# Optimization experiments

Hardware: AMD Instinct MI355X
Metric: run time of the kernel (lower is better)

The kernel has to match this reference:

```python
import jax, jax.numpy as jnp
import numpy as np


def conv1x1(x, w, b):
    # x: [B, Cin, H, W], w: [Cout, Cin], b: [Cout]
    return jnp.einsum('oc,bchw->bohw', w, x) + b[None, :, None, None]


def setup_inputs() -> dict:
    key = jax.random.key(0)
    ks = jax.random.split(key, 10)
    B, C, H, W = 8, 256, 64, 64
    C2 = C // 2
    s = 1.0 / np.sqrt(C)
    s2 = 1.0 / np.sqrt(C2)
    return {
        'x1': jax.random.normal(ks[0], (B, C, H, W), jnp.float32),
        'x2': jax.random.normal(ks[1], (B, C, H, W), jnp.float32),
        'w_th': jax.random.uniform(ks[2], (C2, C), jnp.float32, -s, s),
        'b_th': jax.random.uniform(ks[3], (C2,), jnp.float32, -s, s),
        'w_pi': jax.random.uniform(ks[4], (C2, C), jnp.float32, -s, s),
        'b_pi': jax.random.uniform(ks[5], (C2,), jnp.float32, -s, s),
        'w_g': jax.random.uniform(ks[6], (C2, C), jnp.float32, -s, s),
        'b_g': jax.random.uniform(ks[7], (C2,), jnp.float32, -s, s),
        'w_out': jax.random.uniform(ks[8], (C, C2), jnp.float32, -s2, s2),
        'b_out': jax.random.uniform(ks[9], (C,), jnp.float32, -s2, s2),
    }


def reference(x1, x2, w_th, b_th, w_pi, b_pi, w_g, b_g, w_out, b_out):
    B, C, H, W = x1.shape
    HW = H * W
    res = x1
    # 1x1 conv projections -> [B, C2, HW]
    e1 = conv1x1(x1, w_th, b_th).reshape(B, -1, HW)  # theta
    e2 = conv1x1(x2, w_pi, b_pi).reshape(B, -1, HW)  # phi
    # scores: [B, HW, HW]
    f = jnp.einsum('bcq,bck->bqk', e1, e2)
    # GLOBAL softmax over the whole HWxHW matrix per batch element
    f = jax.nn.softmax(f.reshape(B, HW * HW), axis=1).reshape(B, HW, HW)
    g2 = conv1x1(x2, w_g, b_g).reshape(B, -1, HW)  # [B, C2, HW]
    # out = f @ g2^T -> [B, HW, C2] -> [B, C2, H, W]
    out = jnp.einsum('bqk,bck->bcq', f, g2).reshape(B, -1, H, W)
    out = conv1x1(out, w_out, b_out)
    return out + res
```

## Files before the change

### kernel.cpp

```cpp
#include <hip/hip_runtime.h>

typedef unsigned short u16;
typedef unsigned int u32;
typedef short s16x8 __attribute__((ext_vector_type(8)));
typedef float f32x4 __attribute__((ext_vector_type(4)));

#define HWN 4096
#define CC  256
#define C2  128
#define LOG2E 1.4426950408889634f

static __device__ __forceinline__ u16 f2bf(float f) {
    union { float f; u32 u; } c; c.f = f;
    u32 u = c.u;
    u32 r = (u + 0x7fffu + ((u >> 16) & 1u)) >> 16;
    return (u16)r;
}
static __device__ __forceinline__ float bf2f(u16 u) {
    union { u32 u; float f; } c; c.u = ((u32)u) << 16; return c.f;
}
static __device__ __forceinline__ u32 cvtpk(float lo, float hi) {
    u32 d;
    asm("v_cvt_pk_bf16_f32 %0, %1, %2" : "=v"(d) : "v"(lo), "v"(hi));
    return d;
}
static __device__ __forceinline__ float fexp2(float x) {
    return __builtin_amdgcn_exp2f(x);
}

__global__ __launch_bounds__(256) void k_wcvt(
    const float* __restrict__ w_th, const float* __restrict__ w_pi,
    const float* __restrict__ w_g,  const float* __restrict__ w_out,
    u16* __restrict__ wthb, u16* __restrict__ wpib,
    u16* __restrict__ wgb,  u16* __restrict__ woutb)
{
    int i = blockIdx.x * 256 + threadIdx.x;
    wthb[i]  = f2bf(w_th[i] * LOG2E);
    wpib[i]  = f2bf(w_pi[i]);
    wgb[i]   = f2bf(w_g[i]);
    woutb[i] = f2bf(w_out[i]);
}

__device__ __forceinline__ void load_afrag(const float* __restrict__ px, int g, s16x8 a[8]) {
    #pragma unroll
    for (int ks = 0; ks < 8; ++ks) {
        union { s16x8 v; u16 u[8]; } c;
        #pragma unroll
        for (int j = 0; j < 8; ++j)
            c.u[j] = f2bf(px[(size_t)(ks*32 + g*8 + j) * HWN]);
        a[ks] = c.v;
    }
}

__device__ __forceinline__ void proj_gemm(const s16x8 a[8], const u16* __restrict__ wb,
                                          const float* __restrict__ bias, float bscale,
                                          int m16, int g, f32x4 acc[8]) {
    #pragma unroll
    for (int nb = 0; nb < 8; ++nb) {
        float bv = bias[nb*16 + m16] * bscale;
        acc[nb] = (f32x4){bv, bv, bv, bv};
    }
    #pragma unroll
    for (int ks = 0; ks < 8; ++ks) {
        #pragma unroll
        for (int nb = 0; nb < 8; ++nb) {
            s16x8 bb = *(const s16x8*)&wb[(size_t)(nb*16 + m16)*CC + ks*32 + g*8];
            acc[nb] = __builtin_amdgcn_mfma_f32_16x16x32_bf16(a[ks], bb, acc[nb], 0, 0, 0);
        }
    }
}

__global__ __launch_bounds__(256) void k_projM(
    const float* __restrict__ x1, const float* __restrict__ x2,
    const u16* __restrict__ wthb, const float* __restrict__ b_th,
    const u16* __restrict__ wpib, const float* __restrict__ b_pi,
    const u16* __restrict__ wgb,  const float* __restrict__ b_g,
    u16* __restrict__ e1t, u16* __restrict__ e2t, u16* __restrict__ g2t)
{
    __shared__ u16 gs[C2][72];
    const int tid  = threadIdx.x;
    const int b    = blockIdx.x >> 6;
    const int q0   = (blockIdx.x & 63) * 64;
    const int wid  = __builtin_amdgcn_readfirstlane(tid >> 6);
    const int lane = tid & 63;
    const int m16  = lane & 15;
    const int g    = lane >> 4;

    s16x8 a[8];
    f32x4 acc[8];

    const float* px1 = x1 + (size_t)b*CC*HWN + q0 + wid*16 + m16;
    load_afrag(px1, g, a);
    proj_gemm(a, wthb, b_th, LOG2E, m16, g, acc);
    #pragma unroll
    for (int nb = 0; nb < 8; ++nb)
        #pragma unroll
        for (int r = 0; r < 4; ++r)
            e1t[((size_t)b*HWN + q0 + wid*16 + g*4 + r)*C2 + nb*16 + m16] = f2bf(acc[nb][r]);

    const float* px2 = x2 + (size_t)b*CC*HWN + q0 + wid*16 + m16;
    load_afrag(px2, g, a);
    proj_gemm(a, wpib, b_pi, 1.f, m16, g, acc);
    #pragma unroll
    for (int nb = 0; nb < 8; ++nb)
        #pragma unroll
        for (int r = 0; r < 4; ++r) {
            int q   = q0 + wid*16 + g*4 + r;
            int gix = (nb*2 + (m16 >> 3)) ^ (q & 7);
            e2t[((size_t)b*HWN + q)*C2 + gix*8 + (m16 & 7)] = f2bf(acc[nb][r]);
        }

    proj_gemm(a, wgb, b_g, 1.f, m16, g, acc);
    #pragma unroll
    for (int nb = 0; nb < 8; ++nb)
        #pragma unroll
        for (int r = 0; r < 4; ++r)
            gs[nb*16 + m16][wid*16 + g*4 + r] = f2bf(acc[nb][r]);
    __syncthreads();
    u16* gt = g2t + ((size_t)b*64 + (q0 >> 6))*8192;
    #pragma unroll
    for (int r = 0; r < 4; ++r) {
        int idx = r*256 + tid;
        int row = idx >> 3, c8 = idx & 7;
        union { u16 u[8]; int4 v; } o;
        #pragma unroll
        for (int e = 0; e < 8; ++e) {
            int c  = c8*8 + e;
            int cs = c ^ ((row & 7) << 3);
            int kk = cs >> 5, rem = cs & 31;
            int gg = rem >> 3, jj = rem & 7;
            int ko = kk*32 + ((jj >> 2) << 4) + (gg << 2) + (jj & 3);
            o.u[e] = gs[row][ko];
        }
        *(int4*)&gt[row*64 + c8*8] = o.v;
    }
}

__global__ __launch_bounds__(256, 2) void k_flash(
    const u16* __restrict__ e1t, const u16* __restrict__ e2t,
    const u16* __restrict__ g2t,
    u16* __restrict__ outp0, u16* __restrict__ outp1, float* __restrict__ ms)
{
    __shared__ u16 e2s[128*128];
    __shared__ u16 g2s[2*64*128];

    const int tid  = threadIdx.x;
    const int bid  = ((blockIdx.x & 7) << 6) | (blockIdx.x >> 3);
    const int b    = bid >> 6;
    const int qb   = (bid >> 1) & 31;
    const int seg  = bid & 1;
    const int q0   = qb * 128;
    const int wid  = __builtin_amdgcn_readfirstlane(tid >> 6);
    const int lane = tid & 63;
    const int m16  = lane & 15;
    const int g    = lane >> 4;
    const int sw16 = (m16 & 7) << 3;
    const int phase = ((blockIdx.x >> 3) & 1) * 8;

    s16x8 af[2][4];
    #pragma unroll
    for (int h = 0; h < 2; ++h) {
        const u16* p = e1t + ((size_t)b*HWN + q0 + wid*32 + h*16 + m16)*C2 + g*8;
        #pragma unroll
        for (int kc = 0; kc < 4; ++kc) af[h][kc] = *(const s16x8*)(p + kc*32);
    }

    f32x4 acc[2][8];
    #pragma unroll
    for (int h = 0; h < 2; ++h)
        #pragma unroll
        for (int i = 0; i < 8; ++i) acc[h][i] = (f32x4){0.f,0.f,0.f,0.f};
    f32x4 sacc[2];
    sacc[0] = (f32x4){0.f,0.f,0.f,0.f};
    sacc[1] = (f32x4){0.f,0.f,0.f,0.f};
    union { u16 u[8]; s16x8 v; } onesu;
    #pragma unroll
    for (int i = 0; i < 8; ++i) onesu.u[i] = 0x3F80;
    const s16x8 ones = onesu.v;

    const u16* e2base = e2t + (size_t)b*HWN*C2;
    const u16* g2base = g2t + (size_t)b*64*8192;

    for (int it = 0; it < 16; ++it) {
        const int itp = (it + phase) & 15;
        const int k0  = seg*2048 + itp*128;
        __syncthreads();
        {
            const u16* eG = e2base + (size_t)k0*C2;
            const u16* gG = g2base + (size_t)(k0 >> 6)*8192;
            #pragma unroll
            for (int r = 0; r < 8; ++r) {
                int off = (r*256 + tid)*8;
                int4 ve = *(const int4*)(eG + off);
                int4 vg = *(const int4*)(gG + off);
                *(int4*)&e2s[off] = ve;
                *(int4*)&g2s[off] = vg;
            }
        }
        __syncthreads();

        f32x4 s[2][8];
        #pragma unroll
        for (int h = 0; h < 2; ++h)
            #pragma unroll
            for (int j = 0; j < 8; ++j) s[h][j] = (f32x4){0.f,0.f,0.f,0.f};
        #pragma unroll
        for (int j = 0; j < 8; ++j) {
            #pragma unroll
            for (int kc = 0; kc < 4; ++kc) {
                s16x8 aa = *(const s16x8*)&e2s[((j*16+m16)*128 + kc*32 + g*8) ^ sw16];
                s[0][j] = __builtin_amdgcn_mfma_f32_16x16x32_bf16(aa, af[0][kc], s[0][j], 0, 0, 0);
                s[1][j] = __builtin_amdgcn_mfma_f32_16x16x32_bf16(aa, af[1][kc], s[1][j], 0, 0, 0);
            }
        }

        s16x8 pa[2][4];
        #pragma unroll
        for (int h = 0; h < 2; ++h)
            #pragma unroll
            for (int kk = 0; kk < 4; ++kk) {
                float p0 = fexp2(s[h][2*kk][0]);
                float p1 = fexp2(s[h][2*kk][1]);
                float p2 = fexp2(s[h][2*kk][2]);
                float p3 = fexp2(s[h][2*kk][3]);
                float p4 = fexp2(s[h][2*kk+1][0]);
                float p5 = fexp2(s[h][2*kk+1][1]);
                float p6 = fexp2(s[h][2*kk+1][2]);
                float p7 = fexp2(s[h][2*kk+1][3]);
                union { u32 d[4]; s16x8 v; } pf;
                pf.d[0] = cvtpk(p0, p1);
                pf.d[1] = cvtpk(p2, p3);
                pf.d[2] = cvtpk(p4, p5);
                pf.d[3] = cvtpk(p6, p7);
                pa[h][kk] = pf.v;
            }

        #pragma unroll
        for (int kk = 0; kk < 4; ++kk) {
            const int sub = (kk >> 1) * 8192;
            sacc[0] = __builtin_amdgcn_mfma_f32_16x16x32_bf16(pa[0][kk], ones, sacc[0], 0, 0, 0);
            sacc[1] = __builtin_amdgcn_mfma_f32_16x16x32_bf16(pa[1][kk], ones, sacc[1], 0, 0, 0);
            #pragma unroll
            for (int fc = 0; fc < 8; ++fc) {
                s16x8 gb = *(const s16x8*)&g2s[sub + (fc*16+m16)*64 + (((kk&1)*32 + g*8) ^ sw16)];
                acc[0][fc] = __builtin_amdgcn_mfma_f32_16x16x32_bf16(pa[0][kk], gb, acc[0][fc], 0, 0, 0);
                acc[1][fc] = __builtin_amdgcn_mfma_f32_16x16x32_bf16(pa[1][kk], gb, acc[1][fc], 0, 0, 0);
            }
        }
    }

    float s_w = (sacc[0][0] + sacc[0][1]) + (sacc[0][2] + sacc[0][3])
              + (sacc[1][0] + sacc[1][1]) + (sacc[1][2] + sacc[1][3]);
    #pragma unroll
    for (int off = 32; off >= 1; off >>= 1) s_w += __shfl_xor(s_w, off);
    s_w *= 0.0625f;
    if (lane == 0) {
        int idx = b*256 + seg*128 + qb*4 + wid;
        ms[idx*2 + 0] = 0.f;
        ms[idx*2 + 1] = s_w;
    }
    const float inv_s = 1.f / s_w;
    u16* op = seg ? outp1 : outp0;
    #pragma unroll
    for (int h = 0; h < 2; ++h)
        #pragma unroll
        for (int fc = 0; fc < 8; ++fc)
            #pragma unroll
            for (int r = 0; r < 4; ++r)
                op[((size_t)b*HWN + q0 + wid*32 + h*16 + g*4 + r)*C2 + fc*16 + m16] =
                    f2bf(acc[h][fc][r] * inv_s);
}

__global__ void k_mz(const float* __restrict__ ms, float* __restrict__ mz)
{
    __shared__ float rmax[4], rsum[4];
    const int b = blockIdx.x, tid = threadIdx.x;
    const int lane = tid & 63, wid = tid >> 6;
    float m = ms[((size_t)b*256 + tid)*2 + 0];
    float s = ms[((size_t)b*256 + tid)*2 + 1];
    float mm = m;
    #pragma unroll
    for (int off = 32; off >= 1; off >>= 1) mm = fmaxf(mm, __shfl_xor(mm, off));
    if (lane == 0) rmax[wid] = mm;
    __syncthreads();
    float M = fmaxf(fmaxf(rmax[0], rmax[1]), fmaxf(rmax[2], rmax[3]));
    float z = s * fexp2(m - M);
    #pragma unroll
    for (int off = 32; off >= 1; off >>= 1) z += __shfl_xor(z, off);
    if (lane == 0) rsum[wid] = z;
    __syncthreads();
    if (tid == 0) { mz[b*2] = M; mz[b*2+1] = rsum[0]+rsum[1]+rsum[2]+rsum[3]; }
}

__global__ __launch_bounds__(256) void k_outM(
    const u16* __restrict__ outp0, const u16* __restrict__ outp1,
    const float* __restrict__ ms, const float* __restrict__ mz,
    const u16* __restrict__ woutb, const float* __restrict__ b_out,
    const float* __restrict__ x1, float* __restrict__ out)
{
    const int tid  = threadIdx.x;
    const int b    = blockIdx.x >> 6;
    const int q0   = (blockIdx.x & 63) * 64;
    const int wv   = tid >> 6;
    const int lane = tid & 63;
    const int m16  = lane & 15;
    const int g    = lane >> 4;
    const int q    = q0 + wv*16 + m16;

    const float M    = mz[b*2];
    const float invZ = 1.f / mz[b*2+1];
    const int idx5   = (q0 >> 5) + (wv >> 1);
    const float a0 = ms[(b*256 + idx5)*2+1]       * fexp2(ms[(b*256 + idx5)*2]       - M) * invZ;
    const float a1 = ms[(b*256 + 128 + idx5)*2+1] * fexp2(ms[(b*256 + 128 + idx5)*2] - M) * invZ;

    s16x8 bfr[4];
    #pragma unroll
    for (int ks = 0; ks < 4; ++ks) {
        union { s16x8 v; u16 u[8]; } o0, o1, oc;
        o0.v = *(const s16x8*)&outp0[((size_t)b*HWN + q)*C2 + ks*32 + g*8];
        o1.v = *(const s16x8*)&outp1[((size_t)b*HWN + q)*C2 + ks*32 + g*8];
        #pragma unroll
        for (int j = 0; j < 8; ++j)
            oc.u[j] = f2bf(a0*bf2f(o0.u[j]) + a1*bf2f(o1.u[j]));
        bfr[ks] = oc.v;
    }

    f32x4 acc[16];
    #pragma unroll
    for (int cb = 0; cb < 16; ++cb) acc[cb] = (f32x4){0.f,0.f,0.f,0.f};
    #pragma unroll
    for (int ks = 0; ks < 4; ++ks) {
        #pragma unroll
        for (int cb = 0; cb < 16; ++cb) {
            s16x8 afr = *(const s16x8*)&woutb[(size_t)(cb*16 + m16)*C2 + ks*32 + g*8];
            acc[cb] = __builtin_amdgcn_mfma_f32_16x16x32_bf16(afr, bfr[ks], acc[cb], 0, 0, 0);
        }
    }

    #pragma unroll
    for (int cb = 0; cb < 16; ++cb) {
        f32x4 bb = *(const f32x4*)&b_out[cb*16 + g*4];
        #pragma unroll
        for (int r = 0; r < 4; ++r) {
            int co = cb*16 + g*4 + r;
            size_t o = ((size_t)b*CC + co)*HWN + q;
            out[o] = acc[cb][r] + bb[r] + x1[o];
        }
    }
}

extern "C" void kernel_launch(void* const* d_in, const int* in_sizes, int n_in,
                              void* d_out, int out_size, void* d_ws, size_t ws_size,
                              hipStream_t stream)
{
    const float* x1   = (const float*)d_in[0];
    const float* x2   = (const float*)d_in[1];
    const float* w_th = (const float*)d_in[2];
    const float* b_th = (const float*)d_in[3];
    const float* w_pi = (const float*)d_in[4];
    const float* b_pi = (const float*)d_in[5];
    const float* w_g  = (const float*)d_in[6];
    const float* b_g  = (const float*)d_in[7];
    const float* w_out= (const float*)d_in[8];
    const float* b_out= (const float*)d_in[9];
    float* out = (float*)d_out;

    char* ws = (char*)d_ws;
    u16*   e1t  = (u16*)(ws);
    u16*   e2t  = (u16*)(ws + 8388608);
    u16*   g2t  = (u16*)(ws + 16777216);
    u16*   outp0= (u16*)(ws + 25165824);
    u16*   outp1= (u16*)(ws + 33554432);
    float* ms   = (float*)(ws + 41943040);
    float* mz   = (float*)(ws + 41959424);
    u16*   wthb = (u16*)(ws + 41959488);
    u16*   wpib = (u16*)(ws + 42025024);
    u16*   wgb  = (u16*)(ws + 42090560);
    u16*   woutb= (u16*)(ws + 42156096);

    k_wcvt <<<dim3(128), dim3(256), 0, stream>>>(w_th, w_pi, w_g, w_out, wthb, wpib, wgb, woutb);
    k_projM<<<dim3(512), dim3(256), 0, stream>>>(x1, x2, wthb, b_th, wpib, b_pi, wgb, b_g,
                                                 e1t, e2t, g2t);
    k_flash<<<dim3(512), dim3(256), 0, stream>>>(e1t, e2t, g2t, outp0, outp1, ms);
    k_mz   <<<dim3(8),   dim3(256), 0, stream>>>(ms, mz);
    k_outM <<<dim3(512), dim3(256), 0, stream>>>(outp0, outp1, ms, mz, woutb, b_out, x1, out);
}
```

Before: 177.3 us.

## Split projection kernel per projection and stage inputs via coalesced LDS loads

The projection kernel now launches three times as many blocks, one per projection (theta, phi, g), instead of one block computing all three serially. Each block first loads its 256x64 input tile with coalesced float4 reads, converts it to bf16 in LDS, and then builds MFMA A fragments from LDS. The old path used strided scalar global loads. The aim is more parallelism across CUs and better load coalescing. In exchange, x2 is read twice (once for phi, once for g), and the g-projection path adds an extra barrier so the LDS buffer can be reused.

```diff
diff --git a/kernel.cpp b/kernel.cpp
--- a/kernel.cpp
+++ b/kernel.cpp
@@ -39,17 +39,6 @@
     wpib[i]  = f2bf(w_pi[i]);
     wgb[i]   = f2bf(w_g[i]);
     woutb[i] = f2bf(w_out[i]);
-}
-
-__device__ __forceinline__ void load_afrag(const float* __restrict__ px, int g, s16x8 a[8]) {
-    #pragma unroll
-    for (int ks = 0; ks < 8; ++ks) {
-        union { s16x8 v; u16 u[8]; } c;
-        #pragma unroll
-        for (int j = 0; j < 8; ++j)
-            c.u[j] = f2bf(px[(size_t)(ks*32 + g*8 + j) * HWN]);
-        a[ks] = c.v;
-    }
 }
 
 __device__ __forceinline__ void proj_gemm(const s16x8 a[8], const u16* __restrict__ wb,
@@ -77,62 +66,88 @@
     const u16* __restrict__ wgb,  const float* __restrict__ b_g,
     u16* __restrict__ e1t, u16* __restrict__ e2t, u16* __restrict__ g2t)
 {
-    __shared__ u16 gs[C2][72];
+    __shared__ u16 xs[CC * 68];
     const int tid  = threadIdx.x;
-    const int b    = blockIdx.x >> 6;
-    const int q0   = (blockIdx.x & 63) * 64;
+    const int proj = blockIdx.x >> 9;
+    const int rem  = blockIdx.x & 511;
+    const int b    = rem >> 6;
+    const int q0   = (rem & 63) * 64;
     const int wid  = __builtin_amdgcn_readfirstlane(tid >> 6);
     const int lane = tid & 63;
     const int m16  = lane & 15;
     const int g    = lane >> 4;
+    const int sr   = tid >> 4;
+    const int sq   = (tid & 15) * 4;
+
+    {
+        const float* bx = (proj == 0 ? x1 : x2) + (size_t)b*CC*HWN + q0;
+        #pragma unroll
+        for (int r = 0; r < 16; ++r) {
+            int row = r*16 + sr;
+            float4 v = *(const float4*)(bx + (size_t)row*HWN + sq);
+            uint2 d;
+            d.x = (u32)f2bf(v.x) | ((u32)f2bf(v.y) << 16);
+            d.y = (u32)f2bf(v.z) | ((u32)f2bf(v.w) << 16);
+            *(uint2*)&xs[row*68 + sq] = d;
+        }
+    }
+    __syncthreads();
 
     s16x8 a[8];
+    #pragma unroll
+    for (int ks = 0; ks < 8; ++ks) {
+        union { s16x8 v; u16 u[8]; } c;
+        #pragma unroll
+        for (int j = 0; j < 8; ++j)
+            c.u[j] = xs[(ks*32 + g*8 + j)*68 + wid*16 + m16];
+        a[ks] = c.v;
+    }
+
     f32x4 acc[8];
-
-    const float* px1 = x1 + (size_t)b*CC*HWN + q0 + wid*16 + m16;
-    load_afrag(px1, g, a);
-    proj_gemm(a, wthb, b_th, LOG2E, m16, g, acc);
-    #pragma unroll
-    for (int nb = 0; nb < 8; ++nb)
-        #pragma unroll
-        for (int r = 0; r < 4; ++r)
-            e1t[((size_t)b*HWN + q0 + wid*16 + g*4 + r)*C2 + nb*16 + m16] = f2bf(acc[nb][r]);
-
-    const float* px2 = x2 + (size_t)b*CC*HWN + q0 + wid*16 + m16;
-    load_afrag(px2, g, a);
-    proj_gemm(a, wpib, b_pi, 1.f, m16, g, acc);
-    #pragma unroll
-    for (int nb = 0; nb < 8; ++nb)
+    if (proj == 0) {
+        proj_gemm(a, wthb, b_th, LOG2E, m16, g, acc);
+        #pragma unroll
+        for (int nb = 0; nb < 8; ++nb)
+            #pragma unroll
+            for (int r = 0; r < 4; ++r)
+                e1t[((size_t)b*HWN + q0 + wid*16 + g*4 + r)*C2 + nb*16 + m16] = f2bf(acc[nb][r]);
+    } else if (proj == 1) {
+        proj_gemm(a, wpib, b_pi, 1.f, m16, g, acc);
+        #pragma unroll
+        for (int nb = 0; nb < 8; ++nb)
+            #pragma unroll
+            for (int r = 0; r < 4; ++r) {
+                int q   = q0 + wid*16 + g*4 + r;
+                int gix = (nb*2 + (m16 >> 3)) ^ (q & 7);
+                e2t[((size_t)b*HWN + q)*C2 + gix*8 + (m16 & 7)] = f2bf(acc[nb][r]);
+            }
+    } else {
+        proj_gemm(a, wgb, b_g, 1.f, m16, g, acc);
+        __syncthreads();
+        u16* gs = xs;
+        #pragma unroll
+        for (int nb = 0; nb < 8; ++nb)
+            #pragma unroll
+            for (int r = 0; r < 4; ++r)
+                gs[(nb*16 + m16)*72 + wid*16 + g*4 + r] = f2bf(acc[nb][r]);
+        __syncthreads();
+        u16* gt = g2t + ((size_t)b*64 + (q0 >> 6))*8192;
         #pragma unroll
         for (int r = 0; r < 4; ++r) {
-            int q   = q0 + wid*16 + g*4 + r;
-            int gix = (nb*2 + (m16 >> 3)) ^ (q & 7);
-            e2t[((size_t)b*HWN + q)*C2 + gix*8 + (m16 & 7)] = f2bf(acc[nb][r]);
-        }
-
-    proj_gemm(a, wgb, b_g, 1.f, m16, g, acc);
-    #pragma unroll
-    for (int nb = 0; nb < 8; ++nb)
-        #pragma unroll
-        for (int r = 0; r < 4; ++r)
-            gs[nb*16 + m16][wid*16 + g*4 + r] = f2bf(acc[nb][r]);
-    __syncthreads();
-    u16* gt = g2t + ((size_t)b*64 + (q0 >> 6))*8192;
-    #pragma unroll
-    for (int r = 0; r < 4; ++r) {
-        int idx = r*256 + tid;
-        int row = idx >> 3, c8 = idx & 7;
-        union { u16 u[8]; int4 v; } o;
-        #pragma unroll
-        for (int e = 0; e < 8; ++e) {
-            int c  = c8*8 + e;
-            int cs = c ^ ((row & 7) << 3);
-            int kk = cs >> 5, rem = cs & 31;
-            int gg = rem >> 3, jj = rem & 7;
-            int ko = kk*32 + ((jj >> 2) << 4) + (gg << 2) + (jj & 3);
-            o.u[e] = gs[row][ko];
-        }
-        *(int4*)&gt[row*64 + c8*8] = o.v;
+            int idx = r*256 + tid;
+            int row = idx >> 3, c8 = idx & 7;
+            union { u16 u[8]; int4 v; } o;
+            #pragma unroll
+            for (int e = 0; e < 8; ++e) {
+                int c  = c8*8 + e;
+                int cs = c ^ ((row & 7) << 3);
+                int kk = cs >> 5, rm = cs & 31;
+                int gg = rm >> 3, jj = rm & 7;
+                int ko = kk*32 + ((jj >> 2) << 4) + (gg << 2) + (jj & 3);
+                o.u[e] = gs[row*72 + ko];
+            }
+            *(int4*)&gt[row*64 + c8*8] = o.v;
+        }
     }
 }
 
@@ -378,10 +393,10 @@
     u16*   wgb  = (u16*)(ws + 42090560);
     u16*   woutb= (u16*)(ws + 42156096);
 
-    k_wcvt <<<dim3(128), dim3(256), 0, stream>>>(w_th, w_pi, w_g, w_out, wthb, wpib, wgb, woutb);
-    k_projM<<<dim3(512), dim3(256), 0, stream>>>(x1, x2, wthb, b_th, wpib, b_pi, wgb, b_g,
-                                                 e1t, e2t, g2t);
-    k_flash<<<dim3(512), dim3(256), 0, stream>>>(e1t, e2t, g2t, outp0, outp1, ms);
-    k_mz   <<<dim3(8),   dim3(256), 0, stream>>>(ms, mz);
-    k_outM <<<dim3(512), dim3(256), 0, stream>>>(outp0, outp1, ms, mz, woutb, b_out, x1, out);
-}
+    k_wcvt <<<dim3(128),  dim3(256), 0, stream>>>(w_th, w_pi, w_g, w_out, wthb, wpib, wgb, woutb);
+    k_projM<<<dim3(1536), dim3(256), 0, stream>>>(x1, x2, wthb, b_th, wpib, b_pi, wgb, b_g,
+                                                  e1t, e2t, g2t);
+    k_flash<<<dim3(512),  dim3(256), 0, stream>>>(e1t, e2t, g2t, outp0, outp1, ms);
+    k_mz   <<<dim3(8),    dim3(256), 0, stream>>>(ms, mz);
+    k_outM <<<dim3(512),  dim3(256), 0, stream>>>(outp0, outp1, ms, mz, woutb, b_out, x1, out);
+}
```

Measured after the change: 189.6 us. 7.0% more time.
